# Optimization experiments

Measured on AMD Instinct MI355X. Metric: run time of the kernel, lower is better.

Reference implementation:

```python
import jax, jax.numpy as jnp
import numpy as np
from jax import lax

NUM_CLASSES = 80
NUM_ANCHORS = 9


def _conv(x, w, b):
    # x: [B,C,H,W], w: [O,I,k,k]
    y = lax.conv_general_dilated(x, w, (1, 1), 'SAME',
                                 dimension_numbers=('NCHW', 'OIHW', 'NCHW'))
    return y + b[None, :, None, None]


def _up2(x):
    return jnp.repeat(jnp.repeat(x, 2, axis=2), 2, axis=3)


def _head(x, ws, bs, hw, hb, last_dim):
    for w, b in zip(ws, bs):
        x = jax.nn.relu(_conv(x, w, b))
    x = _conv(x, hw, hb)  # [B, A*last_dim, H, W]
    B = x.shape[0]
    # permute(0,2,3,1).view(B,H,W,A,last_dim).view(B,-1,last_dim)
    return jnp.transpose(x, (0, 2, 3, 1)).reshape(B, -1, last_dim)


def _anchors(img_h, img_w):
    # standard RetinaNet anchors: levels P3-P7, 3 ratios x 3 scales
    ratios = np.array([0.5, 1.0, 2.0])
    scales = np.array([2 ** 0, 2 ** (1.0 / 3.0), 2 ** (2.0 / 3.0)])
    all_a = []
    for lvl in [3, 4, 5, 6, 7]:
        stride = 2 ** lvl
        base = 2 ** (lvl + 2)
        a = np.zeros((9, 4))
        a[:, 2:] = base * np.tile(scales, (2, 3)).T
        areas = a[:, 2] * a[:, 3]
        a[:, 2] = np.sqrt(areas / np.repeat(ratios, 3))
        a[:, 3] = a[:, 2] * np.repeat(ratios, 3)
        a[:, 0::2] -= np.tile(a[:, 2] * 0.5, (2, 1)).T
        a[:, 1::2] -= np.tile(a[:, 3] * 0.5, (2, 1)).T
        fh = (img_h + stride - 1) // stride
        fw = (img_w + stride - 1) // stride
        sx = (np.arange(fw) + 0.5) * stride
        sy = (np.arange(fh) + 0.5) * stride
        SX, SY = np.meshgrid(sx, sy)
        shifts = np.stack([SX.ravel(), SY.ravel(), SX.ravel(), SY.ravel()], axis=1)
        all_a.append((a[None, :, :] + shifts[:, None, :]).reshape(-1, 4))
    return jnp.asarray(np.concatenate(all_a, 0)[None].astype(np.float32))


def setup_inputs() -> dict:
    key = jax.random.key(0)
    ks = iter(jax.random.split(key, 64))

    def rn(shape, scale=1.0):
        return jax.random.normal(next(ks), shape, jnp.float32) * scale

    def cw(o, i, k):
        return rn((o, i, k, k), (2.0 / (i * k * k)) ** 0.5)

    d = {}
    d['c3'] = rn((2, 512, 80, 80))
    d['c4'] = rn((2, 1024, 40, 40))
    d['c5'] = rn((2, 2048, 20, 20))
    d['p6'] = rn((2, 256, 10, 10))
    d['p7'] = rn((2, 256, 5, 5))
    # FPN lateral 1x1 convs and shared top-down 3x3 conv (the source reuses top_down_conv1)
    d['fl1_w'] = cw(256, 2048, 1); d['fl1_b'] = jnp.zeros(256, jnp.float32)
    d['fl2_w'] = cw(256, 1024, 1); d['fl2_b'] = jnp.zeros(256, jnp.float32)
    d['fl3_w'] = cw(256, 512, 1);  d['fl3_b'] = jnp.zeros(256, jnp.float32)
    d['ftd_w'] = cw(256, 256, 3);  d['ftd_b'] = jnp.zeros(256, jnp.float32)
    for i in range(1, 5):
        d['cw%d' % i] = cw(256, 256, 3)
        d['cb%d' % i] = jnp.zeros(256, jnp.float32)
    d['chw'] = cw(NUM_ANCHORS * NUM_CLASSES, 256, 3)
    prior = 0.01
    d['chb'] = jnp.full((NUM_ANCHORS * NUM_CLASSES,), -np.log((1.0 - prior) / prior), jnp.float32)
    for i in range(1, 5):
        d['rw%d' % i] = cw(256, 256, 3)
        d['rb%d' % i] = jnp.zeros(256, jnp.float32)
    d['rhw'] = cw(NUM_ANCHORS * 4, 256, 3)
    d['rhb'] = jnp.zeros(NUM_ANCHORS * 4, jnp.float32)
    return d


def reference(c3, c4, c5, p6, p7,
              fl1_w, fl1_b, fl2_w, fl2_b, fl3_w, fl3_b, ftd_w, ftd_b,
              cw1, cb1, cw2, cb2, cw3, cb3, cw4, cb4, chw, chb,
              rw1, rb1, rw2, rb2, rw3, rb3, rw4, rb4, rhw, rhb):
    # FPN (note: source applies top_down_conv1 to all three levels)
    P5 = _conv(c5, fl1_w, fl1_b)
    P4 = _conv(c4, fl2_w, fl2_b)
    P3 = _conv(c3, fl3_w, fl3_b)
    P4 = _up2(P5) + P4
    P3 = _up2(P4) + P3
    P5 = _conv(P5, ftd_w, ftd_b)
    P4 = _conv(P4, ftd_w, ftd_b)
    P3 = _conv(P3, ftd_w, ftd_b)
    feats = [P3, P4, P5, p6, p7]
    cws, cbs = [cw1, cw2, cw3, cw4], [cb1, cb2, cb3, cb4]
    rws, rbs = [rw1, rw2, rw3, rw4], [rb1, rb2, rb3, rb4]
    classification = jnp.concatenate(
        [_head(f, cws, cbs, chw, chb, NUM_CLASSES) for f in feats], axis=1)
    location = jnp.concatenate(
        [_head(f, rws, rbs, rhw, rhb, 4) for f in feats], axis=1)
    anchors = _anchors(c3.shape[2] * 8, c3.shape[3] * 8)
    return (jax.nn.sigmoid(classification), location, anchors)
```

## Files before the change

### kernel.cpp

```cpp
#include <hip/hip_runtime.h>
#include <math.h>

#define NA_TOT 76725
#define NCLS 80
#define LOC_BASE 12276000
#define ANC_BASE 12889800

typedef short s16x8 __attribute__((ext_vector_type(8)));
typedef short s16x4 __attribute__((ext_vector_type(4)));
typedef float fx4 __attribute__((ext_vector_type(4)));

__device__ __forceinline__ unsigned short f2bf(float f) {
  unsigned u = __float_as_uint(f);
  unsigned r = (u + 0x7FFFu + ((u >> 16) & 1u)) >> 16;
  return (unsigned short)r;
}
__device__ __forceinline__ float bf2f(unsigned short h) {
  return __uint_as_float(((unsigned)h) << 16);
}

__global__ void zk(unsigned short* z) { z[threadIdx.x] = 0; }

__global__ __launch_bounds__(256) void wconv(const float* __restrict__ src, unsigned short* __restrict__ dst,
                                             int O, int Opad, int Cin, int taps, int ncb) {
  int idx = blockIdx.x * 256 + threadIdx.x;
  int tot = taps * ncb * Opad * 32;
  if (idx >= tot) return;
  int c32 = idx & 31;
  int r = idx >> 5;
  int o = r % Opad;
  int q = r / Opad;
  int cb = q % ncb;
  int tp = q / ncb;
  int c = cb * 32 + c32;
  float v = (o < O) ? src[((size_t)o * Cin + c) * taps + tp] : 0.f;
  int cc = ((c32 >> 3) ^ ((o >> 1) & 3)) * 8 + (c32 & 7);
  dst[(size_t)(idx & ~31) + cc] = f2bf(v);
}

__global__ __launch_bounds__(256) void nchw2blk(const float* __restrict__ x, unsigned short* __restrict__ y,
                                                int C, int HW) {
  __shared__ float tile[32][65];
  int pb = blockIdx.x * 64, cb = blockIdx.y, b = blockIdx.z;
  int C32 = C >> 5;
  int t = threadIdx.x;
#pragma unroll
  for (int k = 0; k < 8; ++k) {
    int idx = k * 256 + t;
    int c = idx >> 6, p = idx & 63;
    if (pb + p < HW) tile[c][p] = x[((size_t)b * C + cb * 32 + c) * HW + pb + p];
  }
  __syncthreads();
  int pix = t >> 2, co = (t & 3) * 8;
  if (pb + pix < HW) {
    s16x8 v;
#pragma unroll
    for (int j = 0; j < 8; ++j) v[j] = (short)f2bf(tile[co + j][pix]);
    *(s16x8*)(y + (((size_t)b * C32 + cb) * HW + pb + pix) * 32 + co) = v;
  }
}

__global__ __launch_bounds__(256) void up2add(unsigned short* __restrict__ dst, const unsigned short* __restrict__ src,
                                              int C32, int H, int W) {
  int idx = blockIdx.x * 256 + threadIdx.x;
  int HW = H * W;
  int tot = 2 * C32 * HW * 4;
  if (idx >= tot) return;
  int cv = idx & 3;
  int t = idx >> 2;
  int p = t % HW; t /= HW;
  int cb = t % C32;
  int b = t / C32;
  int h = p / W, w = p - h * W;
  int Hs = H >> 1, Ws = W >> 1;
  size_t di = (((size_t)b * C32 + cb) * HW + p) * 32 + cv * 8;
  size_t si = (((size_t)b * C32 + cb) * (Hs * Ws) + (h >> 1) * Ws + (w >> 1)) * 32 + cv * 8;
  s16x8 d = *(s16x8*)(dst + di);
  s16x8 s = *(const s16x8*)(src + si);
  s16x8 r;
#pragma unroll
  for (int j = 0; j < 8; ++j)
    r[j] = (short)f2bf(bf2f((unsigned short)d[j]) + bf2f((unsigned short)s[j]));
  *(s16x8*)(dst + di) = r;
}

struct LvlParams {
  int nlev;
  int nbcum[6];
  int H[5], W[5], CT[5], RT[5], ncb[5], loff[5];
  const unsigned short* x0[5];
  const unsigned short* x1[5];
  const unsigned short* w0[5];
  const unsigned short* w1[5];
  const float* b0[5];
  const float* b1[5];
  unsigned short* y0[5];
  unsigned short* y1[5];
};

template <int TAPS, int MODE>
__global__ __launch_bounds__(256, 2) void conv_mfma(
    LvlParams P, int Opad, int O, int relu, float* __restrict__ fout,
    const unsigned short* __restrict__ zbuf) {
  constexpr int HO = (TAPS == 9) ? 1 : 0;
  constexpr int CW = 16 + 2 * HO;
  constexpr int NPIX = CW * CW;
  constexpr int NSB = (TAPS == 9) ? 6 : 4;
  constexpr int SLOTS = NSB * 64;
  constexpr int NSA = (TAPS == 9) ? 9 : 1;
  constexpr int AROWS = TAPS * 64;

  int bx = blockIdx.x;
  int L = 0;
  while (L + 1 < P.nlev && bx >= P.nbcum[L + 1]) ++L;
  int nb = bx - P.nbcum[L];
  int H = P.H[L], W = P.W[L], CT = P.CT[L], RT = P.RT[L];
  int ncbL = P.ncb[L];
  int HW = H * W;
  int ct = nb % CT;
  int tmp = nb / CT;
  int rt = tmp % RT;
  int b = tmp / RT;
  int set = blockIdx.z;
  const unsigned short* x = set ? P.x1[L] : P.x0[L];
  const unsigned short* wgt = set ? P.w1[L] : P.w0[L];
  const float* bias = set ? P.b1[L] : P.b0[L];
  unsigned short* y = set ? P.y1[L] : P.y0[L];

  int tid = threadIdx.x;
  int lane = tid & 63, wv = tid >> 6;
  int wn = wv;
  int l15 = lane & 15, l4 = lane >> 4;

  __shared__ unsigned short lds[(AROWS + SLOTS) * 32];
  unsigned short* Abuf = lds;
  unsigned short* Bbuf = lds + AROWS * 32;

  int r0 = rt * 16 - HO, c0 = ct * 16 - HO;
  int obase = blockIdx.y * 64;

  fx4 acc[4][4];
#pragma unroll
  for (int i = 0; i < 4; ++i)
#pragma unroll
    for (int f = 0; f < 4; ++f) acc[i][f] = fx4{0.f, 0.f, 0.f, 0.f};

  auto stageA = [&](int cb) {
#pragma unroll
    for (int s = 0; s < NSA; ++s) {
      int j = wv * NSA + s;
      int t = (TAPS == 9) ? (j >> 2) : 0;
      int q = (TAPS == 9) ? (j & 3) : j;
      const unsigned short* src =
          wgt + (((size_t)t * ncbL + cb) * Opad + obase + q * 16 + (lane >> 2)) * 32 + (lane & 3) * 8;
      unsigned short* dst = Abuf + j * 512;
      __builtin_amdgcn_global_load_lds((const __attribute__((address_space(1))) unsigned int*)src,
                                       (__attribute__((address_space(3))) unsigned int*)dst, 16, 0, 0);
    }
  };

  auto stageB = [&](int cb) {
#pragma unroll
    for (int s = 0; s < NSB; ++s) {
      int ib = wv * (NSB * 16) + s * 16;
      int px = ib + (lane >> 2);
      int hr = px / CW, hc = px - hr * CW;
      int h = r0 + hr, wq = c0 + hc;
      bool ok = (px < NPIX) && (h >= 0) && (h < H) && (wq >= 0) && (wq < W);
      int cs = (lane & 3) ^ ((px >> 1) & 3);
      const unsigned short* src =
          ok ? (x + (((size_t)b * ncbL + cb) * HW + (h * W + wq)) * 32 + cs * 8) : zbuf;
      unsigned short* dst = Bbuf + ib * 32;
      __builtin_amdgcn_global_load_lds((const __attribute__((address_space(1))) unsigned int*)src,
                                       (__attribute__((address_space(3))) unsigned int*)dst, 16, 0, 0);
    }
  };

  for (int cb = 0; cb < ncbL; ++cb) {
    if (cb) __builtin_amdgcn_s_barrier();
    stageA(cb);
    stageB(cb);
    asm volatile("s_waitcnt vmcnt(0)" ::: "memory");
    __builtin_amdgcn_s_barrier();
    __builtin_amdgcn_s_setprio(1);
    if constexpr (TAPS == 9) {
#pragma unroll
      for (int dx = 0; dx < 3; ++dx) {
        s16x8 bw[6];
#pragma unroll
        for (int rr = 0; rr < 6; ++rr) {
          int hpix = (wn * 4 + rr) * CW + (l15 + dx);
          bw[rr] = *(const s16x8*)&Bbuf[hpix * 32 + ((l4 ^ ((hpix >> 1) & 3)) * 8)];
        }
#pragma unroll
        for (int dy = 0; dy < 3; ++dy) {
          const int t = dy * 3 + dx;
          s16x8 a[4];
#pragma unroll
          for (int i = 0; i < 4; ++i)
            a[i] = *(const s16x8*)&Abuf[(t * 64 + i * 16 + l15) * 32 + ((l4 ^ ((l15 >> 1) & 3)) * 8)];
#pragma unroll
          for (int f = 0; f < 4; ++f)
#pragma unroll
            for (int i = 0; i < 4; ++i)
              acc[i][f] = __builtin_amdgcn_mfma_f32_16x16x32_bf16(a[i], bw[f + dy], acc[i][f], 0, 0, 0);
        }
      }
    } else {
      s16x8 a[4];
#pragma unroll
      for (int i = 0; i < 4; ++i)
        a[i] = *(const s16x8*)&Abuf[(i * 16 + l15) * 32 + ((l4 ^ ((l15 >> 1) & 3)) * 8)];
#pragma unroll
      for (int f = 0; f < 4; ++f) {
        int hpix = (wn * 4 + f) * CW + l15;
        s16x8 bfr = *(const s16x8*)&Bbuf[hpix * 32 + ((l4 ^ ((hpix >> 1) & 3)) * 8)];
#pragma unroll
        for (int i = 0; i < 4; ++i)
          acc[i][f] = __builtin_amdgcn_mfma_f32_16x16x32_bf16(a[i], bfr, acc[i][f], 0, 0, 0);
      }
    }
    __builtin_amdgcn_s_setprio(0);
  }

  int r_base = rt * 16 + wn * 4;
  int c_img = ct * 16 + l15;
  if (MODE == 0) {
    int OC32 = gridDim.y * 2;
#pragma unroll
    for (int i = 0; i < 4; ++i) {
      int o0 = obase + i * 16 + l4 * 4;
      fx4 b4 = *(const fx4*)(bias + o0);
#pragma unroll
      for (int f = 0; f < 4; ++f) {
        int r_img = r_base + f;
        if (r_img < H && c_img < W) {
          int p = r_img * W + c_img;
          size_t base = (((size_t)b * OC32 + (o0 >> 5)) * HW + p) * 32 + (o0 & 31);
          s16x4 pk;
#pragma unroll
          for (int j = 0; j < 4; ++j) {
            float v = acc[i][f][j] + b4[j];
            if (relu) v = fmaxf(v, 0.f);
            pk[j] = (short)f2bf(v);
          }
          *(s16x4*)(y + base) = pk;
        }
      }
    }
  } else if (MODE == 1) {
#pragma unroll
    for (int i = 0; i < 4; ++i) {
      int o0 = obase + i * 16 + l4 * 4;
#pragma unroll
      for (int f = 0; f < 4; ++f) {
        int r_img = r_base + f;
        if (r_img < H && c_img < W && o0 < O) {
          int p = r_img * W + c_img;
          int a_ = o0 / NCLS, c0i = o0 - a_ * NCLS;
          size_t n = (size_t)b * NA_TOT + P.loff[L] + (size_t)p * 9 + a_;
          fx4 v;
#pragma unroll
          for (int j = 0; j < 4; ++j)
            v[j] = 1.f / (1.f + __expf(-(acc[i][f][j] + bias[o0 + j])));
          *(fx4*)(fout + n * NCLS + c0i) = v;
        }
      }
    }
  } else {
#pragma unroll
    for (int i = 0; i < 4; ++i) {
      int o0 = obase + i * 16 + l4 * 4;
#pragma unroll
      for (int f = 0; f < 4; ++f) {
        int r_img = r_base + f;
        if (r_img < H && c_img < W && o0 < O) {
          int p = r_img * W + c_img;
          int a_ = o0 >> 2;
          size_t n = (size_t)b * NA_TOT + P.loff[L] + (size_t)p * 9 + a_;
          fx4 v;
#pragma unroll
          for (int j = 0; j < 4; ++j) v[j] = acc[i][f][j] + bias[o0 + j];
          *(fx4*)(fout + n * 4) = v;
        }
      }
    }
  }
}

__global__ __launch_bounds__(256) void anchors_kernel(float* __restrict__ out) {
  int n = blockIdx.x * blockDim.x + threadIdx.x;
  if (n >= NA_TOT) return;
  int rem, fw;
  float stride;
  if (n < 57600)      { rem = n;         fw = 80; stride = 8.f; }
  else if (n < 72000) { rem = n - 57600; fw = 40; stride = 16.f; }
  else if (n < 75600) { rem = n - 72000; fw = 20; stride = 32.f; }
  else if (n < 76500) { rem = n - 75600; fw = 10; stride = 64.f; }
  else                { rem = n - 76500; fw = 5;  stride = 128.f; }
  int k = rem % 9;
  int cell = rem / 9;
  int xg = cell % fw;
  int yg = cell / fw;
  const float scales[3] = {1.f, 1.2599210498948732f, 1.5874010519681994f};
  const float isr[3] = {1.4142135623730951f, 1.f, 0.70710678118654755f};
  const float sr[3]  = {0.70710678118654755f, 1.f, 1.4142135623730951f};
  int si = k % 3, ri = k / 3;
  float base = 4.f * stride;
  float wv = base * scales[si] * isr[ri];
  float hv = base * scales[si] * sr[ri];
  float cx = ((float)xg + 0.5f) * stride;
  float cy = ((float)yg + 0.5f) * stride;
  out[(size_t)n * 4 + 0] = cx - 0.5f * wv;
  out[(size_t)n * 4 + 1] = cy - 0.5f * hv;
  out[(size_t)n * 4 + 2] = cx + 0.5f * wv;
  out[(size_t)n * 4 + 3] = cy + 0.5f * hv;
}

#define W_FL1 0
#define W_FL2 524288
#define W_FL3 786432
#define W_FTD 917504
#define W_CW0 1507328
#define W_RW0 3866624
#define W_CHW 6225920
#define W_RHW 7995392
#define ZBUF_OFF 8290304
#define RA_OFF 8290368
#define P3_OFF 12655168
#define P4_OFF 15931968
#define P5_OFF 16751168
#define T0C_OFF 16955968

static const int TL_OFF[5] = {0, 3276800, 4096000, 4300800, 4352000};

extern "C" void kernel_launch(void* const* d_in, const int* in_sizes, int n_in,
                              void* d_out, int out_size, void* d_ws, size_t ws_size,
                              hipStream_t stream) {
  const float* c3 = (const float*)d_in[0];
  const float* c4 = (const float*)d_in[1];
  const float* c5 = (const float*)d_in[2];
  const float* p6 = (const float*)d_in[3];
  const float* p7 = (const float*)d_in[4];
  const float* flw[3] = {(const float*)d_in[5], (const float*)d_in[7], (const float*)d_in[9]};
  const float* flb[3] = {(const float*)d_in[6], (const float*)d_in[8], (const float*)d_in[10]};
  const float* ftd_w = (const float*)d_in[11];
  const float* ftd_b = (const float*)d_in[12];
  const float* cwf[4] = {(const float*)d_in[13], (const float*)d_in[15], (const float*)d_in[17], (const float*)d_in[19]};
  const float* cbf[4] = {(const float*)d_in[14], (const float*)d_in[16], (const float*)d_in[18], (const float*)d_in[20]};
  const float* chw = (const float*)d_in[21];
  const float* chb = (const float*)d_in[22];
  const float* rwf[4] = {(const float*)d_in[23], (const float*)d_in[25], (const float*)d_in[27], (const float*)d_in[29]};
  const float* rbf[4] = {(const float*)d_in[24], (const float*)d_in[26], (const float*)d_in[28], (const float*)d_in[30]};
  const float* rhw = (const float*)d_in[31];
  const float* rhb = (const float*)d_in[32];

  unsigned short* ws = (unsigned short*)d_ws;
  unsigned short* zbuf = ws + ZBUF_OFF;
  float* out = (float*)d_out;

  unsigned short* ob = (unsigned short*)d_out;
  unsigned short* x3 = ob;
  unsigned short* x4 = ob + 6553600;
  unsigned short* x5 = ob + 9830400;
  unsigned short* t0r = ob;
  unsigned short* t1r = ob + 4364800;
  unsigned short* xp6 = ws + RA_OFF;
  unsigned short* xp7 = ws + RA_OFF + 51200;
  unsigned short* p4l = ws + RA_OFF + 64000;
  unsigned short* p5l = ws + RA_OFF + 883200;
  unsigned short* p3l = ws + RA_OFF + 1088000;
  unsigned short* t1c = ws + RA_OFF;
  unsigned short* t0c = ws + T0C_OFF;
  unsigned short* p3 = ws + P3_OFF;
  unsigned short* p4 = ws + P4_OFF;
  unsigned short* p5 = ws + P5_OFF;

  zk<<<1, 64, 0, stream>>>(zbuf);

  auto wc = [&](const float* s, unsigned short* d, int O, int Opad, int Cin, int taps) {
    int ncb = Cin / 32;
    int tot = taps * ncb * Opad * 32;
    wconv<<<(tot + 255) / 256, 256, 0, stream>>>(s, d, O, Opad, Cin, taps, ncb);
  };
  wc(flw[0], ws + W_FL1, 256, 256, 2048, 1);
  wc(flw[1], ws + W_FL2, 256, 256, 1024, 1);
  wc(flw[2], ws + W_FL3, 256, 256, 512, 1);
  wc(ftd_w, ws + W_FTD, 256, 256, 256, 9);
  for (int k = 0; k < 4; ++k) wc(cwf[k], ws + W_CW0 + k * 589824, 256, 256, 256, 9);
  for (int k = 0; k < 4; ++k) wc(rwf[k], ws + W_RW0 + k * 589824, 256, 256, 256, 9);
  wc(chw, ws + W_CHW, 720, 768, 256, 9);
  wc(rhw, ws + W_RHW, 36, 64, 256, 9);

  nchw2blk<<<dim3(100, 16, 2), 256, 0, stream>>>(c3, x3, 512, 6400);
  nchw2blk<<<dim3(25, 32, 2), 256, 0, stream>>>(c4, x4, 1024, 1600);
  nchw2blk<<<dim3(7, 64, 2), 256, 0, stream>>>(c5, x5, 2048, 400);
  nchw2blk<<<dim3(2, 8, 2), 256, 0, stream>>>(p6, xp6, 256, 100);
  nchw2blk<<<dim3(1, 8, 2), 256, 0, stream>>>(p7, xp7, 256, 25);

  auto fill = [](LvlParams& P, int nlev, const int* Hs) {
    P.nlev = nlev;
    int cum = 0;
    for (int L = 0; L < nlev; ++L) {
      P.nbcum[L] = cum;
      P.H[L] = Hs[L]; P.W[L] = Hs[L];
      P.CT[L] = (Hs[L] + 15) / 16;
      P.RT[L] = (Hs[L] + 15) / 16;
      cum += 2 * P.CT[L] * P.RT[L];
    }
    P.nbcum[nlev] = cum;
  };

  {
    int Hs[3] = {20, 40, 80};
    LvlParams P{};
    fill(P, 3, Hs);
    P.ncb[0] = 64; P.ncb[1] = 32; P.ncb[2] = 16;
    P.x0[0] = x5; P.x0[1] = x4; P.x0[2] = x3;
    P.w0[0] = ws + W_FL1; P.w0[1] = ws + W_FL2; P.w0[2] = ws + W_FL3;
    P.b0[0] = flb[0]; P.b0[1] = flb[1]; P.b0[2] = flb[2];
    P.y0[0] = p5l; P.y0[1] = p4l; P.y0[2] = p3l;
    conv_mfma<1, 0><<<dim3(P.nbcum[3], 4, 1), 256, 0, stream>>>(P, 256, 256, 0, nullptr, zbuf);
  }
  up2add<<<dim3((2 * 8 * 1600 * 4 + 255) / 256), 256, 0, stream>>>(p4l, p5l, 8, 40, 40);
  up2add<<<dim3((2 * 8 * 6400 * 4 + 255) / 256), 256, 0, stream>>>(p3l, p4l, 8, 80, 80);

  {
    int Hs[3] = {80, 40, 20};
    LvlParams P{};
    fill(P, 3, Hs);
    for (int L = 0; L < 3; ++L) {
      P.ncb[L] = 8;
      P.w0[L] = ws + W_FTD;
      P.b0[L] = ftd_b;
    }
    P.x0[0] = p3l; P.x0[1] = p4l; P.x0[2] = p5l;
    P.y0[0] = p3; P.y0[1] = p4; P.y0[2] = p5;
    conv_mfma<9, 0><<<dim3(P.nbcum[3], 4, 1), 256, 0, stream>>>(P, 256, 256, 0, nullptr, zbuf);
  }

  int Hs5[5] = {80, 40, 20, 10, 5};
  int loffs[5] = {0, 57600, 72000, 75600, 76500};
  const unsigned short* feats[5] = {p3, p4, p5, xp6, xp7};

  auto towerP = [&](int layer, const unsigned short* const* xc, const unsigned short* const* xr,
                    unsigned short* yc_base, unsigned short* yr_base) {
    LvlParams P{};
    fill(P, 5, Hs5);
    for (int L = 0; L < 5; ++L) {
      P.ncb[L] = 8;
      P.x0[L] = xc[L];
      P.x1[L] = xr[L];
      P.w0[L] = ws + W_CW0 + layer * 589824;
      P.w1[L] = ws + W_RW0 + layer * 589824;
      P.b0[L] = cbf[layer];
      P.b1[L] = rbf[layer];
      P.y0[L] = yc_base + TL_OFF[L];
      P.y1[L] = yr_base + TL_OFF[L];
    }
    conv_mfma<9, 0><<<dim3(P.nbcum[5], 4, 2), 256, 0, stream>>>(P, 256, 256, 1, nullptr, zbuf);
  };

  const unsigned short* t0c_l[5], *t1c_l[5], *t0r_l[5], *t1r_l[5];
  for (int L = 0; L < 5; ++L) {
    t0c_l[L] = t0c + TL_OFF[L];
    t1c_l[L] = t1c + TL_OFF[L];
    t0r_l[L] = t0r + TL_OFF[L];
    t1r_l[L] = t1r + TL_OFF[L];
  }
  towerP(0, feats, feats, t0c, t0r);
  towerP(1, t0c_l, t0r_l, t1c, t1r);
  towerP(2, t1c_l, t1r_l, t0c, t0r);
  towerP(3, t0c_l, t0r_l, t1c, t1r);

  {
    LvlParams P{};
    fill(P, 5, Hs5);
    for (int L = 0; L < 5; ++L) {
      P.ncb[L] = 8;
      P.x0[L] = t1r_l[L];
      P.w0[L] = ws + W_RHW;
      P.b0[L] = rhb;
      P.loff[L] = loffs[L];
    }
    conv_mfma<9, 2><<<dim3(P.nbcum[5], 1, 1), 256, 0, stream>>>(P, 64, 36, 0, out + LOC_BASE, zbuf);
  }
  {
    LvlParams P{};
    fill(P, 5, Hs5);
    for (int L = 0; L < 5; ++L) {
      P.ncb[L] = 8;
      P.x0[L] = t1c_l[L];
      P.w0[L] = ws + W_CHW;
      P.b0[L] = chb;
      P.loff[L] = loffs[L];
    }
    conv_mfma<9, 1><<<dim3(P.nbcum[5], 12, 1), 256, 0, stream>>>(P, 768, 720, 0, out, zbuf);
  }

  anchors_kernel<<<dim3((NA_TOT + 255) / 256), 256, 0, stream>>>(out + ANC_BASE);
}
```

Measured before the change: 445.0 us.

## Double-buffer activation tiles in LDS to overlap loads with MFMA

Splits the B (activation) LDS buffer into two slots so the next channel block's activations are prefetched with global_load_lds while MFMAs run on the current slot. Weights (A) are still loaded after compute under barriers. It also trims per-wave B slot counts so waves 1-3 load 5 slots instead of 6 for 3x3 convs, cutting padding loads. LDS usage grows, which may reduce occupancy below the 2-blocks-per-CU launch bound, and the A load still serializes each iteration.

Measured after the change: 450.3 us. About the same (+1.2%).

```diff
diff --git a/kernel.cpp b/kernel.cpp
--- a/kernel.cpp
+++ b/kernel.cpp
@@ -105,8 +105,9 @@
   constexpr int HO = (TAPS == 9) ? 1 : 0;
   constexpr int CW = 16 + 2 * HO;
   constexpr int NPIX = CW * CW;
-  constexpr int NSB = (TAPS == 9) ? 6 : 4;
-  constexpr int SLOTS = NSB * 64;
+  constexpr int NSB0 = (TAPS == 9) ? 6 : 4;
+  constexpr int NSB1 = (TAPS == 9) ? 5 : 4;
+  constexpr int BSLOT = (NSB0 + 3 * NSB1) * 16;
   constexpr int NSA = (TAPS == 9) ? 9 : 1;
   constexpr int AROWS = TAPS * 64;
 
@@ -132,7 +133,7 @@
   int wn = wv;
   int l15 = lane & 15, l4 = lane >> 4;
 
-  __shared__ unsigned short lds[(AROWS + SLOTS) * 32];
+  __shared__ unsigned short lds[(AROWS + 2 * BSLOT) * 32];
   unsigned short* Abuf = lds;
   unsigned short* Bbuf = lds + AROWS * 32;
 
@@ -159,29 +160,35 @@
     }
   };
 
-  auto stageB = [&](int cb) {
-#pragma unroll
-    for (int s = 0; s < NSB; ++s) {
-      int ib = wv * (NSB * 16) + s * 16;
-      int px = ib + (lane >> 2);
-      int hr = px / CW, hc = px - hr * CW;
-      int h = r0 + hr, wq = c0 + hc;
-      bool ok = (px < NPIX) && (h >= 0) && (h < H) && (wq >= 0) && (wq < W);
-      int cs = (lane & 3) ^ ((px >> 1) & 3);
-      const unsigned short* src =
-          ok ? (x + (((size_t)b * ncbL + cb) * HW + (h * W + wq)) * 32 + cs * 8) : zbuf;
-      unsigned short* dst = Bbuf + ib * 32;
-      __builtin_amdgcn_global_load_lds((const __attribute__((address_space(1))) unsigned int*)src,
-                                       (__attribute__((address_space(3))) unsigned int*)dst, 16, 0, 0);
+  auto stageB = [&](unsigned short* Bb, int cb) {
+    int nsw = (wv == 0) ? NSB0 : NSB1;
+    int base = (wv == 0) ? 0 : (NSB0 + (wv - 1) * NSB1) * 16;
+#pragma unroll
+    for (int s = 0; s < NSB0; ++s) {
+      if (s < nsw) {
+        int ib = base + s * 16;
+        int px = ib + (lane >> 2);
+        int hr = px / CW, hc = px - hr * CW;
+        int h = r0 + hr, wq = c0 + hc;
+        bool ok = (px < NPIX) && (h >= 0) && (h < H) && (wq >= 0) && (wq < W);
+        int cs = (lane & 3) ^ ((px >> 1) & 3);
+        const unsigned short* src =
+            ok ? (x + (((size_t)b * ncbL + cb) * HW + (h * W + wq)) * 32 + cs * 8) : zbuf;
+        unsigned short* dst = Bb + ib * 32;
+        __builtin_amdgcn_global_load_lds((const __attribute__((address_space(1))) unsigned int*)src,
+                                         (__attribute__((address_space(3))) unsigned int*)dst, 16, 0, 0);
+      }
     }
   };
 
+  stageA(0);
+  stageB(Bbuf, 0);
+  asm volatile("s_waitcnt vmcnt(0)" ::: "memory");
+  __builtin_amdgcn_s_barrier();
+
   for (int cb = 0; cb < ncbL; ++cb) {
-    if (cb) __builtin_amdgcn_s_barrier();
-    stageA(cb);
-    stageB(cb);
-    asm volatile("s_waitcnt vmcnt(0)" ::: "memory");
-    __builtin_amdgcn_s_barrier();
+    unsigned short* Bcur = Bbuf + (size_t)(cb & 1) * BSLOT * 32;
+    if (cb + 1 < ncbL) stageB(Bbuf + (size_t)((cb + 1) & 1) * BSLOT * 32, cb + 1);
     __builtin_amdgcn_s_setprio(1);
     if constexpr (TAPS == 9) {
 #pragma unroll
@@ -190,7 +197,7 @@
 #pragma unroll
         for (int rr = 0; rr < 6; ++rr) {
           int hpix = (wn * 4 + rr) * CW + (l15 + dx);
-          bw[rr] = *(const s16x8*)&Bbuf[hpix * 32 + ((l4 ^ ((hpix >> 1) & 3)) * 8)];
+          bw[rr] = *(const s16x8*)&Bcur[hpix * 32 + ((l4 ^ ((hpix >> 1) & 3)) * 8)];
         }
 #pragma unroll
         for (int dy = 0; dy < 3; ++dy) {
@@ -214,13 +221,19 @@
 #pragma unroll
       for (int f = 0; f < 4; ++f) {
         int hpix = (wn * 4 + f) * CW + l15;
-        s16x8 bfr = *(const s16x8*)&Bbuf[hpix * 32 + ((l4 ^ ((hpix >> 1) & 3)) * 8)];
+        s16x8 bfr = *(const s16x8*)&Bcur[hpix * 32 + ((l4 ^ ((hpix >> 1) & 3)) * 8)];
 #pragma unroll
         for (int i = 0; i < 4; ++i)
           acc[i][f] = __builtin_amdgcn_mfma_f32_16x16x32_bf16(a[i], bfr, acc[i][f], 0, 0, 0);
       }
     }
     __builtin_amdgcn_s_setprio(0);
+    if (cb + 1 < ncbL) {
+      __builtin_amdgcn_s_barrier();
+      stageA(cb + 1);
+      asm volatile("s_waitcnt vmcnt(0)" ::: "memory");
+      __builtin_amdgcn_s_barrier();
+    }
   }
 
   int r_base = rt * 16 + wn * 4;
```
